# Kernel optimization log

Hardware: AMD Instinct MI355X
Metric: run time of the kernel (lower is better)

## Reference

```python
import jax, jax.numpy as jnp
import numpy as np

B, S, D, H, F = 2, 2048, 1024, 16, 4096
DH = D // H
EPS = 1e-6


def setup_inputs() -> dict:
    key = jax.random.key(0)
    ks = jax.random.split(key, 8)
    x = jax.random.normal(ks[0], (B, S, D), dtype=jnp.float32)
    # causal mask, broadcastable over [B,H,S,S]
    attention_mask = jnp.tril(jnp.ones((S, S), dtype=bool))[None, None]
    Wqkv = jax.random.normal(ks[1], (3 * D, D), dtype=jnp.float32) * (1.0 / np.sqrt(D))
    Wout = jax.random.normal(ks[2], (D, D), dtype=jnp.float32) * (1.0 / np.sqrt(D))
    W1 = jax.random.normal(ks[3], (F, D), dtype=jnp.float32) * (1.0 / np.sqrt(D))
    b1 = jnp.zeros((F,), dtype=jnp.float32)
    W2 = jax.random.normal(ks[4], (D, F), dtype=jnp.float32) * (1.0 / np.sqrt(F))
    b2 = jnp.zeros((D,), dtype=jnp.float32)
    gamma1 = jnp.ones((D,), dtype=jnp.float32)
    beta1 = jnp.zeros((D,), dtype=jnp.float32)
    gamma2 = jnp.ones((D,), dtype=jnp.float32)
    beta2 = jnp.zeros((D,), dtype=jnp.float32)
    return {"x": x, "attention_mask": attention_mask, "Wqkv": Wqkv, "Wout": Wout,
            "W1": W1, "b1": b1, "W2": W2, "b2": b2,
            "gamma1": gamma1, "beta1": beta1, "gamma2": gamma2, "beta2": beta2}


def layer_norm(x, gamma, beta):
    # Matches torch module: (x - mean) / (std + eps), std unbiased=False
    mean = jnp.mean(x, axis=-1, keepdims=True)
    std = jnp.sqrt(jnp.mean((x - mean) ** 2, axis=-1, keepdims=True))
    return gamma * ((x - mean) / (std + EPS)) + beta


def reference(x, attention_mask, Wqkv, Wout, W1, b1, W2, b2, gamma1, beta1, gamma2, beta2):
    # --- attention sub-block (Pre-LN) ---
    h = layer_norm(x, gamma1, beta1)
    qkv = h @ Wqkv.T                                   # [B,S,3D]
    qkv = qkv.reshape(B, S, 3, H, DH).transpose(2, 0, 3, 1, 4)  # [3,B,H,S,DH]
    q, k, v = qkv[0], qkv[1], qkv[2]
    scale = DH ** -0.5
    scores = jnp.einsum('bhqd,bhkd->bhqk', q, k) * scale
    scores = jnp.where(attention_mask, scores, -jnp.inf)
    attn = jax.nn.softmax(scores, axis=-1)
    out = jnp.einsum('bhqk,bhkd->bhqd', attn, v)       # [B,H,S,DH]
    out = out.transpose(0, 2, 1, 3).reshape(B, S, D)
    out = out @ Wout.T
    x = x + out                                        # dropout eval = identity
    # --- FFN sub-block (Pre-LN) ---
    h = layer_norm(x, gamma2, beta2)
    h = jax.nn.gelu(h @ W1.T + b1, approximate=False)  # torch GELU default = exact erf
    h = h @ W2.T + b2
    return x + h
```

## Files before the change

kernel.cpp:

```cpp
#include <hip/hip_runtime.h>
#include <hip/hip_bf16.h>
#include <math.h>


typedef __bf16 bf16;
typedef __bf16 bf16x4 __attribute__((ext_vector_type(4)));
typedef __bf16 bf16x8 __attribute__((ext_vector_type(8)));
typedef float f32x4 __attribute__((ext_vector_type(4)));

#define LOG2E 1.4426950408889634f
#define NSHIFT -17.312340489f

__device__ __forceinline__ f32x4 mfma16(bf16x8 a, bf16x8 b, f32x4 c) {
    return __builtin_amdgcn_mfma_f32_16x16x32_bf16(a, b, c, 0, 0, 0);
}
__device__ __forceinline__ void load16_lds(const bf16* g, bf16* l) {
    __builtin_amdgcn_global_load_lds(
        (__attribute__((address_space(1))) void*)g,
        (__attribute__((address_space(3))) void*)l, 16, 0, 0);
}

__global__ __launch_bounds__(256) void cvt_kernel(const float* __restrict__ in,
                                                  bf16* __restrict__ out, int n) {
    const int i = (blockIdx.x * 256 + threadIdx.x) * 4;
    if (i < n) {
        const float4 f = *(const float4*)(in + i);
        bf16x4 o;
        o[0] = (bf16)f.x; o[1] = (bf16)f.y; o[2] = (bf16)f.z; o[3] = (bf16)f.w;
        *(bf16x4*)(out + i) = o;
    }
}

__global__ __launch_bounds__(256) void ln_kernel(const float* __restrict__ xin,
                                                 bf16* __restrict__ out,
                                                 const float* __restrict__ gamma,
                                                 const float* __restrict__ beta) {
    const int row = blockIdx.x;
    const int tid = threadIdx.x;
    const float4 f = *(const float4*)(xin + (size_t)row * 1024 + tid * 4);
    float v[4] = {f.x, f.y, f.z, f.w};
    float s = v[0] + v[1] + v[2] + v[3];
    float s2 = v[0] * v[0] + v[1] * v[1] + v[2] * v[2] + v[3] * v[3];
#pragma unroll
    for (int off = 1; off < 64; off <<= 1) {
        s += __shfl_xor(s, off);
        s2 += __shfl_xor(s2, off);
    }
    __shared__ float red[8];
    const int wave = tid >> 6, lane = tid & 63;
    if (lane == 0) { red[wave] = s; red[4 + wave] = s2; }
    __syncthreads();
    s = red[0] + red[1] + red[2] + red[3];
    s2 = red[4] + red[5] + red[6] + red[7];
    const float mean = s * (1.0f / 1024.0f);
    float var = s2 * (1.0f / 1024.0f) - mean * mean;
    var = fmaxf(var, 0.0f);
    const float rstd = 1.0f / (sqrtf(var) + 1e-6f);
    const int c = tid * 4;
    const float4 g = *(const float4*)(gamma + c);
    const float4 b = *(const float4*)(beta + c);
    bf16x4 o;
    o[0] = (bf16)((v[0] - mean) * rstd * g.x + b.x);
    o[1] = (bf16)((v[1] - mean) * rstd * g.y + b.y);
    o[2] = (bf16)((v[2] - mean) * rstd * g.z + b.z);
    o[3] = (bf16)((v[3] - mean) * rstd * g.w + b.w);
    *(bf16x4*)(out + (size_t)row * 1024 + c) = o;
}

template <int EPI>
__global__ __launch_bounds__(256) void gemm_bt(const bf16* __restrict__ A,
                                               const bf16* __restrict__ B,
                                               int N, int K, int ldk,
                                               bf16* __restrict__ outb,
                                               float* __restrict__ outf,
                                               const float* __restrict__ bias,
                                               const float* __restrict__ resf,
                                               bf16* __restrict__ qk,
                                               bf16* __restrict__ vt) {
    __shared__ alignas(16) bf16 As[128 * 32];
    __shared__ alignas(16) bf16 Bs[128 * 32];
    const int tid = threadIdx.x;
    const int bm = blockIdx.x, bn = blockIdx.y;
    const int wave = tid >> 6, lane = tid & 63;
    const int wm = (wave >> 1) * 64, wn = (wave & 1) * 64;
    const int l16 = lane & 15, quad = lane >> 4;

    f32x4 acc[4][4] = {};

    const size_t koff = (size_t)blockIdx.z * K;
    const int row0 = tid >> 2, ch0 = tid & 3;
    const int gch = ch0 ^ ((row0 >> 1) & 3);
    const bf16* Ap = A + (size_t)(bm * 128 + row0) * ldk + koff + gch * 8;
    const bf16* Bp = B + (size_t)(bn * 128 + row0) * ldk + koff + gch * 8;
    bf16* AsP = &As[tid * 8];
    bf16* BsP = &Bs[tid * 8];
    const size_t rstep = (size_t)64 * ldk;

    for (int k0 = 0; k0 < K; k0 += 32) {
#pragma unroll
        for (int r = 0; r < 2; r++) {
            load16_lds(Ap + r * rstep + k0, AsP + r * 2048);
            load16_lds(Bp + r * rstep + k0, BsP + r * 2048);
        }
        __syncthreads();
        bf16x8 af[4], bfr[4];
#pragma unroll
        for (int i = 0; i < 4; i++) {
            const int ra = wm + i * 16 + l16;
            af[i] = *(const bf16x8*)(&As[ra * 32 + (quad ^ ((ra >> 1) & 3)) * 8]);
        }
#pragma unroll
        for (int j = 0; j < 4; j++) {
            const int rb = wn + j * 16 + l16;
            bfr[j] = *(const bf16x8*)(&Bs[rb * 32 + (quad ^ ((rb >> 1) & 3)) * 8]);
        }
#pragma unroll
        for (int i = 0; i < 4; i++)
#pragma unroll
            for (int j = 0; j < 4; j++) acc[i][j] = mfma16(af[i], bfr[j], acc[i][j]);
        __syncthreads();
    }

#pragma unroll
    for (int i = 0; i < 4; i++) {
#pragma unroll
        for (int j = 0; j < 4; j++) {
            const int gr0 = bm * 128 + wm + i * 16 + quad * 4;
            const int gc = bn * 128 + wn + j * 16 + l16;
            float bv = 0.0f;
            if (EPI == 2) bv = bias[gc];
            if (EPI == 5 && bias && blockIdx.z == 0) bv = bias[gc];
            if (EPI == 4 && gc >= 2048) {
                const int n = gc - 2048;
                const int hh = n >> 6, dd = n & 63;
                const int bb = gr0 >> 11, ss = gr0 & 2047;
                bf16x4 pk;
#pragma unroll
                for (int r = 0; r < 4; r++) pk[r] = (bf16)acc[i][j][r];
                *(bf16x4*)(vt + ((size_t)((bb * 16 + hh) * 64 + dd)) * 2048 + ss) = pk;
            } else {
#pragma unroll
                for (int r = 0; r < 4; r++) {
                    const float v = acc[i][j][r];
                    const size_t idx = (size_t)(gr0 + r) * N + gc;
                    if (EPI == 0) {
                        outb[idx] = (bf16)v;
                    } else if (EPI == 1) {
                        outf[idx] = v + resf[idx];
                    } else if (EPI == 2) {
                        const float t = v + bv;
                        outb[idx] = (bf16)(0.5f * t * (1.0f + erff(t * 0.70710678118654752f)));
                    } else if (EPI == 5) {
                        atomicAdd(&outf[idx], v + bv);
                    } else {
                        qk[(size_t)(gr0 + r) * 2048 + gc] = (bf16)v;
                    }
                }
            }
        }
    }
}

__global__ __launch_bounds__(256, 4) void flash_attn(const bf16* __restrict__ qk,
                                                     const bf16* __restrict__ vt,
                                                     bf16* __restrict__ attn) {
    __shared__ alignas(16) bf16 Ks[64 * 72];
    __shared__ alignas(16) bf16 Vs[64 * 72];
    __shared__ alignas(16) bf16 Ps[4][16 * 72];
    const int tid = threadIdx.x;
    const int wave = tid >> 6, lane = tid & 63;
    const int l16 = lane & 15, quad = lane >> 4;
    const int bh = blockIdx.x;
    const int qt = 31 - blockIdx.y;
    const int b = bh >> 4, h = bh & 15;
    const int q0w = qt * 64 + wave * 16;
    const bf16* qkb = qk + (size_t)b * 2048 * 2048;
    const bf16* vtb = vt + (size_t)bh * 64 * 2048;

    bf16x8 qf[2];
#pragma unroll
    for (int c = 0; c < 2; c++) {
        bf16x8 v = *(const bf16x8*)(qkb + (size_t)(q0w + l16) * 2048 +
                                    h * 64 + c * 32 + quad * 8);
#pragma unroll
        for (int e = 0; e < 8; e++) v[e] = (bf16)((float)v[e] * 0.125f);
        qf[c] = v;
    }

    float lsum[4] = {0.0f, 0.0f, 0.0f, 0.0f};
    f32x4 o[4] = {};

    const int ntiles = qt + 1;
    for (int t = 0; t < ntiles; t++) {
        const int k0 = t * 64;
#pragma unroll
        for (int i = 0; i < 2; i++) {
            const int r = i * 32 + (tid >> 3), ch = tid & 7;
            *(uint4*)(&Ks[r * 72 + ch * 8]) =
                *(const uint4*)(qkb + (size_t)(k0 + r) * 2048 + 1024 + h * 64 + ch * 8);
            *(uint4*)(&Vs[r * 72 + ch * 8]) =
                *(const uint4*)(vtb + (size_t)r * 2048 + k0 + ch * 8);
        }
        __syncthreads();
        f32x4 s[4];
#pragma unroll
        for (int kt = 0; kt < 4; kt++) {
            const bf16x8 k0f = *(const bf16x8*)(&Ks[(kt * 16 + l16) * 72 + quad * 8]);
            const bf16x8 k1f = *(const bf16x8*)(&Ks[(kt * 16 + l16) * 72 + 32 + quad * 8]);
            s[kt] = mfma16(qf[1], k1f, mfma16(qf[0], k0f, (f32x4){0, 0, 0, 0}));
        }
        const bool need_mask = (t == ntiles - 1);
#pragma unroll
        for (int r = 0; r < 4; r++) {
            const int qrow = q0w + quad * 4 + r;
            float e0 = exp2f(fmaf(s[0][r], LOG2E, NSHIFT));
            float e1 = exp2f(fmaf(s[1][r], LOG2E, NSHIFT));
            float e2 = exp2f(fmaf(s[2][r], LOG2E, NSHIFT));
            float e3 = exp2f(fmaf(s[3][r], LOG2E, NSHIFT));
            if (need_mask) {
                if (k0 + l16 > qrow) e0 = 0.0f;
                if (k0 + 16 + l16 > qrow) e1 = 0.0f;
                if (k0 + 32 + l16 > qrow) e2 = 0.0f;
                if (k0 + 48 + l16 > qrow) e3 = 0.0f;
            }
            lsum[r] += (e0 + e1) + (e2 + e3);
            bf16* pp = &Ps[wave][(quad * 4 + r) * 72];
            pp[l16] = (bf16)e0;
            pp[16 + l16] = (bf16)e1;
            pp[32 + l16] = (bf16)e2;
            pp[48 + l16] = (bf16)e3;
        }
#pragma unroll
        for (int c = 0; c < 2; c++) {
            const bf16x8 pf = *(const bf16x8*)(&Ps[wave][l16 * 72 + c * 32 + quad * 8]);
#pragma unroll
            for (int dt = 0; dt < 4; dt++) {
                const bf16x8 vf =
                    *(const bf16x8*)(&Vs[(dt * 16 + l16) * 72 + c * 32 + quad * 8]);
                o[dt] = mfma16(pf, vf, o[dt]);
            }
        }
        __syncthreads();
    }

#pragma unroll
    for (int r = 0; r < 4; r++) {
#pragma unroll
        for (int off = 1; off < 16; off <<= 1) lsum[r] += __shfl_xor(lsum[r], off);
        lsum[r] = 1.0f / fmaxf(lsum[r], 1e-30f);
    }
    bf16* ob = attn + (size_t)b * 2048 * 1024;
#pragma unroll
    for (int dt = 0; dt < 4; dt++)
#pragma unroll
        for (int r = 0; r < 4; r++) {
            const int q = q0w + quad * 4 + r;
            ob[(size_t)q * 1024 + h * 64 + dt * 16 + l16] = (bf16)(o[dt][r] * lsum[r]);
        }
}

extern "C" void kernel_launch(void* const* d_in, const int* in_sizes, int n_in,
                              void* d_out, int out_size, void* d_ws, size_t ws_size,
                              hipStream_t stream) {
    const float* x    = (const float*)d_in[0];
    const float* Wqkv = (const float*)d_in[2];
    const float* Wout = (const float*)d_in[3];
    const float* W1   = (const float*)d_in[4];
    const float* b1   = (const float*)d_in[5];
    const float* W2   = (const float*)d_in[6];
    const float* b2   = (const float*)d_in[7];
    const float* g1   = (const float*)d_in[8];
    const float* be1  = (const float*)d_in[9];
    const float* g2   = (const float*)d_in[10];
    const float* be2  = (const float*)d_in[11];

    char* ws = (char*)d_ws;
    bf16* Wqkv_b = (bf16*)(ws);
    bf16* Wout_b = (bf16*)(ws + (6u << 20));
    bf16* W1_b   = (bf16*)(ws + (8u << 20));
    bf16* W2_b   = (bf16*)(ws + (16u << 20));
    bf16* h      = (bf16*)(ws + (24u << 20));
    bf16* qkbuf  = (bf16*)(ws + (32u << 20));
    bf16* vtbuf  = (bf16*)(ws + (48u << 20));
    bf16* attn   = (bf16*)(ws + (56u << 20));
    bf16* act    = (bf16*)(ws + (32u << 20));
    float* x2    = (float*)d_out;

    cvt_kernel<<<3072, 256, 0, stream>>>(Wqkv, Wqkv_b, 3072 * 1024);
    cvt_kernel<<<1024, 256, 0, stream>>>(Wout, Wout_b, 1024 * 1024);
    cvt_kernel<<<4096, 256, 0, stream>>>(W1, W1_b, 4096 * 1024);
    cvt_kernel<<<4096, 256, 0, stream>>>(W2, W2_b, 4096 * 1024);

    ln_kernel<<<4096, 256, 0, stream>>>(x, h, g1, be1);
    gemm_bt<4><<<dim3(32, 24), 256, 0, stream>>>(h, Wqkv_b, 3072, 1024, 1024,
                                                 nullptr, nullptr, nullptr, nullptr,
                                                 qkbuf, vtbuf);
    flash_attn<<<dim3(32, 32), 256, 0, stream>>>(qkbuf, vtbuf, attn);
    gemm_bt<1><<<dim3(32, 8), 256, 0, stream>>>(attn, Wout_b, 1024, 1024, 1024,
                                                nullptr, x2, nullptr, x, nullptr, nullptr);
    ln_kernel<<<4096, 256, 0, stream>>>(x2, h, g2, be2);
    gemm_bt<2><<<dim3(32, 32), 256, 0, stream>>>(h, W1_b, 4096, 1024, 1024,
                                                 act, nullptr, b1, nullptr, nullptr, nullptr);
    gemm_bt<5><<<dim3(32, 8, 2), 256, 0, stream>>>(act, W2_b, 1024, 2048, 4096,
                                                   nullptr, x2, b2, nullptr, nullptr, nullptr);
}
```

Measured before the change: 412.7 us.

## Double-buffer GEMM LDS tiles and merge weight conversions into one kernel

The GEMM main loop now uses two LDS buffers for A and B. It issues the global-to-LDS loads for the next K-slice before running the MFMAs on the current slice, so memory latency can overlap with compute, and it drops one barrier per iteration. An occupancy hint of 3 blocks per CU is added to the launch bounds. The four separate fp32-to-bf16 weight conversion launches are folded into one launch that picks the source by block index, which removes launch overhead. The cost is twice the LDS per block, which may reduce how many blocks fit on a CU.

```diff
diff --git a/kernel.cpp b/kernel.cpp
--- a/kernel.cpp
+++ b/kernel.cpp
@@ -20,15 +20,23 @@
         (__attribute__((address_space(3))) void*)l, 16, 0, 0);
 }
 
-__global__ __launch_bounds__(256) void cvt_kernel(const float* __restrict__ in,
-                                                  bf16* __restrict__ out, int n) {
-    const int i = (blockIdx.x * 256 + threadIdx.x) * 4;
-    if (i < n) {
-        const float4 f = *(const float4*)(in + i);
-        bf16x4 o;
-        o[0] = (bf16)f.x; o[1] = (bf16)f.y; o[2] = (bf16)f.z; o[3] = (bf16)f.w;
-        *(bf16x4*)(out + i) = o;
-    }
+__global__ __launch_bounds__(256) void cvt4_kernel(const float* __restrict__ s0,
+                                                   const float* __restrict__ s1,
+                                                   const float* __restrict__ s2,
+                                                   const float* __restrict__ s3,
+                                                   bf16* __restrict__ dst) {
+    const int blk = blockIdx.x;
+    const float* s;
+    int base;
+    if (blk < 3072)      { s = s0; base = blk * 1024; }
+    else if (blk < 4096) { s = s1; base = (blk - 3072) * 1024; }
+    else if (blk < 8192) { s = s2; base = (blk - 4096) * 1024; }
+    else                 { s = s3; base = (blk - 8192) * 1024; }
+    const int t4 = threadIdx.x * 4;
+    const float4 f = *(const float4*)(s + base + t4);
+    bf16x4 o;
+    o[0] = (bf16)f.x; o[1] = (bf16)f.y; o[2] = (bf16)f.z; o[3] = (bf16)f.w;
+    *(bf16x4*)(dst + (size_t)blk * 1024 + t4) = o;
 }
 
 __global__ __launch_bounds__(256) void ln_kernel(const float* __restrict__ xin,
@@ -68,17 +76,17 @@
 }
 
 template <int EPI>
-__global__ __launch_bounds__(256) void gemm_bt(const bf16* __restrict__ A,
-                                               const bf16* __restrict__ B,
-                                               int N, int K, int ldk,
-                                               bf16* __restrict__ outb,
-                                               float* __restrict__ outf,
-                                               const float* __restrict__ bias,
-                                               const float* __restrict__ resf,
-                                               bf16* __restrict__ qk,
-                                               bf16* __restrict__ vt) {
-    __shared__ alignas(16) bf16 As[128 * 32];
-    __shared__ alignas(16) bf16 Bs[128 * 32];
+__global__ __launch_bounds__(256, 3) void gemm_bt(const bf16* __restrict__ A,
+                                                  const bf16* __restrict__ B,
+                                                  int N, int K, int ldk,
+                                                  bf16* __restrict__ outb,
+                                                  float* __restrict__ outf,
+                                                  const float* __restrict__ bias,
+                                                  const float* __restrict__ resf,
+                                                  bf16* __restrict__ qk,
+                                                  bf16* __restrict__ vt) {
+    __shared__ alignas(16) bf16 As[2][128 * 32];
+    __shared__ alignas(16) bf16 Bs[2][128 * 32];
     const int tid = threadIdx.x;
     const int bm = blockIdx.x, bn = blockIdx.y;
     const int wave = tid >> 6, lane = tid & 63;
@@ -92,27 +100,34 @@
     const int gch = ch0 ^ ((row0 >> 1) & 3);
     const bf16* Ap = A + (size_t)(bm * 128 + row0) * ldk + koff + gch * 8;
     const bf16* Bp = B + (size_t)(bn * 128 + row0) * ldk + koff + gch * 8;
-    bf16* AsP = &As[tid * 8];
-    bf16* BsP = &Bs[tid * 8];
     const size_t rstep = (size_t)64 * ldk;
 
-    for (int k0 = 0; k0 < K; k0 += 32) {
-#pragma unroll
-        for (int r = 0; r < 2; r++) {
-            load16_lds(Ap + r * rstep + k0, AsP + r * 2048);
-            load16_lds(Bp + r * rstep + k0, BsP + r * 2048);
-        }
-        __syncthreads();
+#pragma unroll
+    for (int r = 0; r < 2; r++) {
+        load16_lds(Ap + r * rstep, &As[0][tid * 8 + r * 2048]);
+        load16_lds(Bp + r * rstep, &Bs[0][tid * 8 + r * 2048]);
+    }
+    __syncthreads();
+
+    int buf = 0;
+    for (int k0 = 0; k0 < K; k0 += 32, buf ^= 1) {
+        if (k0 + 32 < K) {
+#pragma unroll
+            for (int r = 0; r < 2; r++) {
+                load16_lds(Ap + r * rstep + k0 + 32, &As[buf ^ 1][tid * 8 + r * 2048]);
+                load16_lds(Bp + r * rstep + k0 + 32, &Bs[buf ^ 1][tid * 8 + r * 2048]);
+            }
+        }
         bf16x8 af[4], bfr[4];
 #pragma unroll
         for (int i = 0; i < 4; i++) {
             const int ra = wm + i * 16 + l16;
-            af[i] = *(const bf16x8*)(&As[ra * 32 + (quad ^ ((ra >> 1) & 3)) * 8]);
+            af[i] = *(const bf16x8*)(&As[buf][ra * 32 + (quad ^ ((ra >> 1) & 3)) * 8]);
         }
 #pragma unroll
         for (int j = 0; j < 4; j++) {
             const int rb = wn + j * 16 + l16;
-            bfr[j] = *(const bf16x8*)(&Bs[rb * 32 + (quad ^ ((rb >> 1) & 3)) * 8]);
+            bfr[j] = *(const bf16x8*)(&Bs[buf][rb * 32 + (quad ^ ((rb >> 1) & 3)) * 8]);
         }
 #pragma unroll
         for (int i = 0; i < 4; i++)
@@ -275,6 +290,7 @@
     const float* be2  = (const float*)d_in[11];
 
     char* ws = (char*)d_ws;
+    bf16* Wb     = (bf16*)(ws);
     bf16* Wqkv_b = (bf16*)(ws);
     bf16* Wout_b = (bf16*)(ws + (6u << 20));
     bf16* W1_b   = (bf16*)(ws + (8u << 20));
@@ -286,10 +302,7 @@
     bf16* act    = (bf16*)(ws + (32u << 20));
     float* x2    = (float*)d_out;
 
-    cvt_kernel<<<3072, 256, 0, stream>>>(Wqkv, Wqkv_b, 3072 * 1024);
-    cvt_kernel<<<1024, 256, 0, stream>>>(Wout, Wout_b, 1024 * 1024);
-    cvt_kernel<<<4096, 256, 0, stream>>>(W1, W1_b, 4096 * 1024);
-    cvt_kernel<<<4096, 256, 0, stream>>>(W2, W2_b, 4096 * 1024);
+    cvt4_kernel<<<12288, 256, 0, stream>>>(Wqkv, Wout, W1, W2, Wb);
 
     ln_kernel<<<4096, 256, 0, stream>>>(x, h, g1, be1);
     gemm_bt<4><<<dim3(32, 24), 256, 0, stream>>>(h, Wqkv_b, 3072, 1024, 1024,
```

After: 380.1 us. 7.9% less time.
